# Optimization experiments

Hardware: AMD Instinct MI355X
Metric: run time of the kernel (lower is better)

Reference implementation:

```python
import jax, jax.numpy as jnp
import numpy as np

TOP_K = 2  # num_experts_per_token


def setup_inputs() -> dict:
    key = jax.random.key(0)
    k1, k2, k3, k4 = jax.random.split(key, 4)
    B, S, D, F, E = 2, 2048, 1024, 4096, 8
    hidden_states = jax.random.normal(k1, (B, S, D), dtype=jnp.float32)
    # router: nn.Linear(D, E, bias=False) -> weight [E, D]
    Wr = jax.random.normal(k2, (E, D), dtype=jnp.float32) * (1.0 / np.sqrt(D))
    # expert FFNs: W1 [E, D, F] (first Linear, transposed), W2 [E, F, D]
    W1 = jax.random.normal(k3, (E, D, F), dtype=jnp.float32) * (1.0 / np.sqrt(D))
    W2 = jax.random.normal(k4, (E, F, D), dtype=jnp.float32) * (1.0 / np.sqrt(F))
    return {"hidden_states": hidden_states, "Wr": Wr, "W1": W1, "W2": W2}


def reference(hidden_states, Wr, W1, W2):
    B, S, D = hidden_states.shape
    E = Wr.shape[0]
    x = hidden_states.reshape(-1, D)                      # [T, D]
    T = x.shape[0]

    router_logits = x @ Wr.T                              # [T, E]
    routing_weights = jax.nn.softmax(router_logits, axis=-1)
    top_w, top_idx = jax.lax.top_k(routing_weights, TOP_K)  # [T, K]
    top_w = top_w / jnp.sum(top_w, axis=-1, keepdims=True)

    # combine weights scattered into dense [T, E] (zero for unselected experts)
    comb = jnp.zeros((T, E), dtype=x.dtype).at[
        jnp.arange(T)[:, None], top_idx
    ].add(top_w)

    # per-expert FFN: SiLU(x @ W1) @ W2, computed densely then masked-combined
    h = jax.nn.silu(jnp.einsum('td,edf->tef', x, W1))     # [T, E, F]
    y = jnp.einsum('tef,efd->ted', h, W2)                 # [T, E, D]
    out = jnp.einsum('te,ted->td', comb, y)               # [T, D]
    return out.reshape(B, S, D)
```

## Files before the change

kernel.cpp:

```cpp
#include <hip/hip_runtime.h>
#include <hip/hip_bf16.h>

#define T_TOK 4096
#define DDIM  1024
#define FDIM  4096
#define NEXP  8
#define TLMAX 72

typedef __attribute__((ext_vector_type(8))) short bf16x8;
typedef __attribute__((ext_vector_type(4))) float f32x4;

__device__ __forceinline__ void gl2lds16(const void* g, void* l) {
  __builtin_amdgcn_global_load_lds((const __attribute__((address_space(1))) void*)g,
                                   (__attribute__((address_space(3))) void*)l,
                                   16, 0, 0);
}

__device__ __forceinline__ unsigned short f2bf(float f) {
  unsigned u = __float_as_uint(f);
  unsigned r = (u + 0x7fffu + ((u >> 16) & 1u)) >> 16;
  return (unsigned short)r;
}
__device__ __forceinline__ float bf2f(unsigned short u) {
  return __uint_as_float((unsigned)u << 16);
}

__global__ __launch_bounds__(256) void moe_router(
    const float* __restrict__ x, const float* __restrict__ Wr,
    unsigned short* __restrict__ xb, int* __restrict__ te, float* __restrict__ tw) {
  __shared__ float wr[NEXP * DDIM];
  const int tid = threadIdx.x;
#pragma unroll
  for (int i = 0; i < NEXP * DDIM / 256; ++i) wr[i * 256 + tid] = Wr[i * 256 + tid];
  __syncthreads();

  const int wave = tid >> 6, lane = tid & 63;
  const int t = blockIdx.x * 4 + wave;
  const float* xr = x + (size_t)t * DDIM;
  const int d0 = lane * 16;

  float4 xv[4];
#pragma unroll
  for (int j = 0; j < 4; ++j) xv[j] = *(const float4*)(xr + d0 + j * 4);

  float lg[NEXP];
#pragma unroll
  for (int e = 0; e < NEXP; ++e) {
    float s = 0.f;
#pragma unroll
    for (int j = 0; j < 4; ++j) {
      float4 wv = *(const float4*)(&wr[e * DDIM + d0 + j * 4]);
      s += xv[j].x * wv.x + xv[j].y * wv.y + xv[j].z * wv.z + xv[j].w * wv.w;
    }
    lg[e] = s;
  }
#pragma unroll
  for (int e = 0; e < NEXP; ++e) {
#pragma unroll
    for (int off = 32; off > 0; off >>= 1) lg[e] += __shfl_xor(lg[e], off);
  }

#pragma unroll
  for (int j = 0; j < 4; ++j) {
    ushort4 o;
    o.x = f2bf(xv[j].x); o.y = f2bf(xv[j].y); o.z = f2bf(xv[j].z); o.w = f2bf(xv[j].w);
    *(ushort4*)(xb + (size_t)t * DDIM + d0 + j * 4) = o;
  }

  if (lane == 0) {
    int i0 = 0;
#pragma unroll
    for (int e = 1; e < NEXP; ++e) if (lg[e] > lg[i0]) i0 = e;
    int i1 = (i0 == 0) ? 1 : 0;
#pragma unroll
    for (int e = 0; e < NEXP; ++e) if (e != i0 && lg[e] > lg[i1]) i1 = e;
    float w0 = 1.f / (1.f + __expf(lg[i1] - lg[i0]));
    te[t * 2 + 0] = i0; te[t * 2 + 1] = i1;
    tw[t * 2 + 0] = w0; tw[t * 2 + 1] = 1.f - w0;
  }
}

__global__ __launch_bounds__(256) void moe_count(const int* __restrict__ te,
                                                 int* __restrict__ counts) {
  __shared__ int lh[NEXP];
  const int tid = threadIdx.x;
  if (tid < NEXP) lh[tid] = 0;
  __syncthreads();
  const int t = blockIdx.x * 256 + tid;
  atomicAdd(&lh[te[t * 2 + 0]], 1);
  atomicAdd(&lh[te[t * 2 + 1]], 1);
  __syncthreads();
  if (tid < NEXP) atomicAdd(&counts[tid], lh[tid]);
}

__global__ void moe_prefix(const int* __restrict__ counts, int* __restrict__ offs,
                           int* __restrict__ fill, int* __restrict__ tcnt,
                           int* __restrict__ tlist) {
  if (threadIdx.x == 0) {
    int s = 0, tt = 0;
    for (int e = 0; e < NEXP; ++e) {
      offs[e] = s;
      int c = counts[e];
      s += c;
      fill[e] = 0;
      for (int mt = 0; mt * 128 < c; ++mt) tlist[tt++] = (e << 8) | mt;
    }
    offs[NEXP] = s;
    tcnt[0] = tt;
  }
}

__global__ __launch_bounds__(256) void moe_scatter(
    const int* __restrict__ te, const int* __restrict__ offs, int* __restrict__ fill,
    int* __restrict__ rows, int* __restrict__ slot) {
  __shared__ int lcnt[NEXP], lbase[NEXP];
  const int tid = threadIdx.x;
  if (tid < NEXP) lcnt[tid] = 0;
  __syncthreads();
  const int t = blockIdx.x * 256 + tid;
  const int e0 = te[t * 2 + 0], e1 = te[t * 2 + 1];
  const int r0 = atomicAdd(&lcnt[e0], 1);
  const int r1 = atomicAdd(&lcnt[e1], 1);
  __syncthreads();
  if (tid < NEXP) lbase[tid] = atomicAdd(&fill[tid], lcnt[tid]);
  __syncthreads();
  int p0 = offs[e0] + lbase[e0] + r0;
  int p1 = offs[e1] + lbase[e1] + r1;
  rows[p0] = t; rows[p1] = t;
  slot[t * 2 + 0] = p0; slot[t * 2 + 1] = p1;
}

__global__ __launch_bounds__(256) void wconv_t(const float* __restrict__ W,
                                               unsigned short* __restrict__ Wt,
                                               int K, int N) {
  __shared__ unsigned short t[64][65];
  const int e = blockIdx.z;
  const float* src = W + (size_t)e * K * N + (size_t)(blockIdx.y * 64) * N + blockIdx.x * 64;
  unsigned short* dst = Wt + (size_t)e * N * K + (size_t)(blockIdx.x * 64) * K + blockIdx.y * 64;
  const int tid = threadIdx.x;
  const int rr = tid >> 4;
  const int cc4 = (tid & 15) * 4;
#pragma unroll
  for (int i = 0; i < 4; ++i) {
    int r = i * 16 + rr;
    float4 v = *(const float4*)(src + (size_t)r * N + cc4);
    t[cc4 + 0][r] = f2bf(v.x);
    t[cc4 + 1][r] = f2bf(v.y);
    t[cc4 + 2][r] = f2bf(v.z);
    t[cc4 + 3][r] = f2bf(v.w);
  }
  __syncthreads();
  const int k8 = (tid & 7) * 8;
#pragma unroll
  for (int i = 0; i < 2; ++i) {
    int c = i * 32 + (tid >> 3);
    uint4 pk;
    pk.x = (unsigned)t[c][k8 + 0] | ((unsigned)t[c][k8 + 1] << 16);
    pk.y = (unsigned)t[c][k8 + 2] | ((unsigned)t[c][k8 + 3] << 16);
    pk.z = (unsigned)t[c][k8 + 4] | ((unsigned)t[c][k8 + 5] << 16);
    pk.w = (unsigned)t[c][k8 + 6] | ((unsigned)t[c][k8 + 7] << 16);
    *(uint4*)(dst + (size_t)c * K + k8) = pk;
  }
}

template <int KD, int KSLICE, int ND, bool GATHER, bool DOSILU>
__global__ __launch_bounds__(512, 4) void moe_gemm(
    const unsigned short* __restrict__ Asrc, const unsigned short* __restrict__ Wt,
    const int* __restrict__ rows, const int* __restrict__ offs,
    const int* __restrict__ tcnt, const int* __restrict__ tlist,
    unsigned short* __restrict__ Out) {
  constexpr int BM = 128, BN = 256, BK = 32;
  constexpr int S = KD / KSLICE;
  constexpr int NTN = ND / BN;
  constexpr int NPAN = NTN * S;
  constexpr int NB = TLMAX * NPAN;
  constexpr int MF = 4, NF = 4;

  __shared__ alignas(16) unsigned short Alds[2][BM * BK];
  __shared__ alignas(16) unsigned short Blds[2][BN * BK];

  const int bid = blockIdx.x;
  const int orig = (bid & 7) * (NB >> 3) + (bid >> 3);
  const int TT = tcnt[0];
  if (orig >= TT * NPAN) return;
  const int tt = orig % TT;
  const int panel = orig / TT;
  const int nt = panel % NTN;
  const int ksl = panel / NTN;
  const int pk = tlist[tt];
  const int e = pk >> 8, mt = pk & 255;

  const int base = offs[e];
  const int cnt = offs[e + 1] - base;
  const int m0 = mt * BM;
  const int valid = min(BM, cnt - m0);
  const size_t koff = (size_t)ksl * KSLICE;

  const int tid = threadIdx.x;
  const int w = tid >> 6, lane = tid & 63;
  const int wm = w >> 2, wn = w & 3;

  const int n0 = nt * BN;
  const unsigned short* Wb = Wt + (size_t)e * ND * KD + (size_t)n0 * KD + koff;

  const int cc8 = (((tid & 3) ^ ((tid >> 3) & 3)) * 8);
  const int ar = tid >> 2;
  const int aslot = base + m0 + min(ar, valid - 1);
  const size_t aoff = (size_t)(GATHER ? rows[aslot] : aslot) * KD + koff + cc8;
  size_t boff[2];
#pragma unroll
  for (int s = 0; s < 2; ++s) boff[s] = (size_t)(s * 128 + ar) * KD + cc8;

  f32x4 acc[MF][NF] = {};

#define STAGE(b, k0)                                                         \
  {                                                                          \
    gl2lds16(Asrc + aoff + (k0), &Alds[b][tid * 8]);                         \
    _Pragma("unroll") for (int s = 0; s < 2; ++s)                            \
        gl2lds16(Wb + boff[s] + (k0), &Blds[b][(s * 512 + tid) * 8]);        \
  }

#define COMPUTE(b)                                                           \
  {                                                                          \
    bf16x8 af[MF], bfr[NF];                                                  \
    _Pragma("unroll") for (int mf = 0; mf < MF; ++mf) {                      \
      int row = wm * 64 + mf * 16 + (lane & 15);                             \
      int cc = (lane >> 4) ^ ((row >> 1) & 3);                               \
      af[mf] = *(const bf16x8*)((const char*)&Alds[b][0] + row * 64 + cc * 16); \
    }                                                                        \
    _Pragma("unroll") for (int nf = 0; nf < NF; ++nf) {                      \
      int col = wn * 64 + nf * 16 + (lane & 15);                             \
      int cc = (lane >> 4) ^ ((col >> 1) & 3);                               \
      bfr[nf] = *(const bf16x8*)((const char*)&Blds[b][0] + col * 64 + cc * 16); \
    }                                                                        \
    _Pragma("unroll") for (int mf = 0; mf < MF; ++mf)                        \
        _Pragma("unroll") for (int nf = 0; nf < NF; ++nf)                    \
            acc[mf][nf] = __builtin_amdgcn_mfma_f32_16x16x32_bf16(           \
                af[mf], bfr[nf], acc[mf][nf], 0, 0, 0);                      \
  }

  constexpr int NK = KSLICE / BK;
  STAGE(0, 0);
  for (int t = 0; t < NK; t += 2) {
    STAGE(1, (t + 1) * BK);
    asm volatile("s_waitcnt vmcnt(3)" ::: "memory");
    __builtin_amdgcn_s_barrier();
    COMPUTE(0);
    __builtin_amdgcn_s_barrier();
    if (t + 2 < NK) {
      STAGE(0, (t + 2) * BK);
      asm volatile("s_waitcnt vmcnt(3)" ::: "memory");
    } else {
      asm volatile("s_waitcnt vmcnt(0)" ::: "memory");
    }
    __builtin_amdgcn_s_barrier();
    COMPUTE(1);
    __builtin_amdgcn_s_barrier();
  }
#undef STAGE
#undef COMPUTE

  unsigned short* Op = Out + (size_t)ksl * 8192 * ND;
  const int q = lane >> 4, c16 = lane & 15;
#pragma unroll
  for (int mf = 0; mf < MF; ++mf) {
#pragma unroll
    for (int r = 0; r < 4; ++r) {
      int lrow = wm * 64 + mf * 16 + q * 4 + r;
      if (lrow < valid) {
#pragma unroll
        for (int nf = 0; nf < NF; ++nf) {
          int gcol = n0 + wn * 64 + nf * 16 + c16;
          float v = acc[mf][nf][r];
          if (DOSILU) v = v / (1.f + __expf(-v));
          Op[(size_t)(base + m0 + lrow) * ND + gcol] = f2bf(v);
        }
      }
    }
  }
}

__global__ __launch_bounds__(256) void moe_combine(
    const unsigned short* __restrict__ y, const int* __restrict__ slot,
    const float* __restrict__ tw, float* __restrict__ out) {
  const int t = blockIdx.x;
  const int s0 = slot[t * 2], s1 = slot[t * 2 + 1];
  const float w0 = tw[t * 2], w1 = tw[t * 2 + 1];
  const int i = threadIdx.x * 4;
  ushort4 a = *(const ushort4*)(y + (size_t)s0 * DDIM + i);
  ushort4 b = *(const ushort4*)(y + (size_t)(8192 + s0) * DDIM + i);
  ushort4 c = *(const ushort4*)(y + (size_t)s1 * DDIM + i);
  ushort4 d = *(const ushort4*)(y + (size_t)(8192 + s1) * DDIM + i);
  float4 r;
  r.x = w0 * (bf2f(a.x) + bf2f(b.x)) + w1 * (bf2f(c.x) + bf2f(d.x));
  r.y = w0 * (bf2f(a.y) + bf2f(b.y)) + w1 * (bf2f(c.y) + bf2f(d.y));
  r.z = w0 * (bf2f(a.z) + bf2f(b.z)) + w1 * (bf2f(c.z) + bf2f(d.z));
  r.w = w0 * (bf2f(a.w) + bf2f(b.w)) + w1 * (bf2f(c.w) + bf2f(d.w));
  *(float4*)(out + (size_t)t * DDIM + i) = r;
}

extern "C" void kernel_launch(void* const* d_in, const int* in_sizes, int n_in,
                              void* d_out, int out_size, void* d_ws, size_t ws_size,
                              hipStream_t stream) {
  const float* x  = (const float*)d_in[0];
  const float* Wr = (const float*)d_in[1];
  const float* W1 = (const float*)d_in[2];
  const float* W2 = (const float*)d_in[3];
  float* out = (float*)d_out;

  char* ws = (char*)d_ws;
  unsigned short* xb = (unsigned short*)ws;
  unsigned short* H  = (unsigned short*)(ws + (size_t)(8 << 20));
  unsigned short* WT = (unsigned short*)(ws + (size_t)(72 << 20));
  unsigned short* y  = (unsigned short*)(ws + (size_t)(136 << 20));
  char* meta = ws + (size_t)(168 << 20);
  int* rows   = (int*)meta;
  int* te     = (int*)(meta + (32 << 10));
  float* tw   = (float*)(meta + (64 << 10));
  int* slot   = (int*)(meta + (96 << 10));
  int* counts = (int*)(meta + (128 << 10));
  int* offs   = counts + 16;
  int* fill   = counts + 32;
  int* tcnt   = counts + 48;
  int* tlist  = counts + 64;

  hipMemsetAsync(counts, 0, 256, stream);

  moe_router<<<T_TOK / 4, 256, 0, stream>>>(x, Wr, xb, te, tw);
  moe_count<<<T_TOK / 256, 256, 0, stream>>>(te, counts);
  moe_prefix<<<1, 64, 0, stream>>>(counts, offs, fill, tcnt, tlist);
  moe_scatter<<<T_TOK / 256, 256, 0, stream>>>(te, offs, fill, rows, slot);

  wconv_t<<<dim3(FDIM / 64, DDIM / 64, NEXP), 256, 0, stream>>>(W1, WT, DDIM, FDIM);
  moe_gemm<DDIM, DDIM, FDIM, true, true>
      <<<TLMAX * (FDIM / 256), 512, 0, stream>>>(xb, WT, rows, offs, tcnt, tlist, H);

  wconv_t<<<dim3(DDIM / 64, FDIM / 64, NEXP), 256, 0, stream>>>(W2, WT, FDIM, DDIM);
  moe_gemm<FDIM, FDIM / 2, DDIM, false, false>
      <<<TLMAX * (DDIM / 256) * 2, 512, 0, stream>>>(H, WT, nullptr, offs, tcnt, tlist, y);

  moe_combine<<<T_TOK, 256, 0, stream>>>(y, slot, tw, out);
}
```

Before: 318.7 us.

## Deepen MoE GEMM LDS pipeline to four stages with interleaved prefetch

Replaces the double-buffered LDS pipeline with a four-slot ring buffer, processing two BK=32 sub-tiles per loop iteration. Each phase loads its fragments, issues the next global-to-LDS prefetch, then runs the MFMAs at raised wave priority. The LDS swizzle is changed to a three-term XOR to reduce bank conflicts. Occupancy hint drops from 4 to 2 blocks per CU because LDS use doubles, trading latency hiding across blocks for deeper prefetch within a block.

```diff
diff --git a/kernel.cpp b/kernel.cpp
--- a/kernel.cpp
+++ b/kernel.cpp
@@ -164,20 +164,20 @@
 }
 
 template <int KD, int KSLICE, int ND, bool GATHER, bool DOSILU>
-__global__ __launch_bounds__(512, 4) void moe_gemm(
+__global__ __launch_bounds__(512, 2) void moe_gemm(
     const unsigned short* __restrict__ Asrc, const unsigned short* __restrict__ Wt,
     const int* __restrict__ rows, const int* __restrict__ offs,
     const int* __restrict__ tcnt, const int* __restrict__ tlist,
     unsigned short* __restrict__ Out) {
-  constexpr int BM = 128, BN = 256, BK = 32;
+  constexpr int BM = 128, BN = 256;
+  constexpr int NK = KSLICE / 64;
   constexpr int S = KD / KSLICE;
   constexpr int NTN = ND / BN;
   constexpr int NPAN = NTN * S;
   constexpr int NB = TLMAX * NPAN;
-  constexpr int MF = 4, NF = 4;
-
-  __shared__ alignas(16) unsigned short Alds[2][BM * BK];
-  __shared__ alignas(16) unsigned short Blds[2][BN * BK];
+
+  __shared__ alignas(16) unsigned short Ards[4 * BM * 32];
+  __shared__ alignas(16) unsigned short Brds[4 * BN * 32];
 
   const int bid = blockIdx.x;
   const int orig = (bid & 7) * (NB >> 3) + (bid >> 3);
@@ -203,7 +203,7 @@
   const int n0 = nt * BN;
   const unsigned short* Wb = Wt + (size_t)e * ND * KD + (size_t)n0 * KD + koff;
 
-  const int cc8 = (((tid & 3) ^ ((tid >> 3) & 3)) * 8);
+  const int cc8 = (((tid & 3) ^ ((tid >> 2) & 3) ^ ((tid >> 4) & 3)) * 8);
   const int ar = tid >> 2;
   const int aslot = base + m0 + min(ar, valid - 1);
   const size_t aoff = (size_t)(GATHER ? rows[aslot] : aslot) * KD + koff + cc8;
@@ -211,65 +211,65 @@
 #pragma unroll
   for (int s = 0; s < 2; ++s) boff[s] = (size_t)(s * 128 + ar) * KD + cc8;
 
-  f32x4 acc[MF][NF] = {};
-
-#define STAGE(b, k0)                                                         \
-  {                                                                          \
-    gl2lds16(Asrc + aoff + (k0), &Alds[b][tid * 8]);                         \
-    _Pragma("unroll") for (int s = 0; s < 2; ++s)                            \
-        gl2lds16(Wb + boff[s] + (k0), &Blds[b][(s * 512 + tid) * 8]);        \
-  }
-
-#define COMPUTE(b)                                                           \
-  {                                                                          \
-    bf16x8 af[MF], bfr[NF];                                                  \
-    _Pragma("unroll") for (int mf = 0; mf < MF; ++mf) {                      \
-      int row = wm * 64 + mf * 16 + (lane & 15);                             \
-      int cc = (lane >> 4) ^ ((row >> 1) & 3);                               \
-      af[mf] = *(const bf16x8*)((const char*)&Alds[b][0] + row * 64 + cc * 16); \
-    }                                                                        \
-    _Pragma("unroll") for (int nf = 0; nf < NF; ++nf) {                      \
-      int col = wn * 64 + nf * 16 + (lane & 15);                             \
-      int cc = (lane >> 4) ^ ((col >> 1) & 3);                               \
-      bfr[nf] = *(const bf16x8*)((const char*)&Blds[b][0] + col * 64 + cc * 16); \
-    }                                                                        \
-    _Pragma("unroll") for (int mf = 0; mf < MF; ++mf)                        \
-        _Pragma("unroll") for (int nf = 0; nf < NF; ++nf)                    \
-            acc[mf][nf] = __builtin_amdgcn_mfma_f32_16x16x32_bf16(           \
-                af[mf], bfr[nf], acc[mf][nf], 0, 0, 0);                      \
-  }
-
-  constexpr int NK = KSLICE / BK;
-  STAGE(0, 0);
+  const int kgp = (lane >> 4) ^ (lane & 3) ^ ((lane >> 2) & 3);
+  const int aro = (wm * 64 + (lane & 15)) * 64 + kgp * 16;
+  const int bro = (wn * 64 + (lane & 15)) * 64 + kgp * 16;
+
+  f32x4 acc[4][4] = {};
+
+#define SA(sl, ke) gl2lds16(Asrc + aoff + (ke), Ards + (sl)*4096 + tid * 8)
+#define SB(sl, ke, s) gl2lds16(Wb + boff[s] + (ke), Brds + (sl)*8192 + ((s)*512 + tid) * 8)
+
+#define PHASE(sl, STG)                                                        \
+  {                                                                           \
+    bf16x8 af[4], bfr[4];                                                     \
+    const char* Ab = (const char*)Ards + (sl) * 8192 + aro;                   \
+    const char* Bb = (const char*)Brds + (sl) * 16384 + bro;                  \
+    _Pragma("unroll") for (int mf = 0; mf < 4; ++mf)                          \
+        af[mf] = *(const bf16x8*)(Ab + mf * 1024);                            \
+    _Pragma("unroll") for (int nf = 0; nf < 4; ++nf)                          \
+        bfr[nf] = *(const bf16x8*)(Bb + nf * 1024);                           \
+    STG;                                                                      \
+    asm volatile("s_waitcnt vmcnt(6)" ::: "memory");                          \
+    __builtin_amdgcn_s_barrier();                                             \
+    __builtin_amdgcn_s_setprio(1);                                            \
+    _Pragma("unroll") for (int mf = 0; mf < 4; ++mf)                          \
+        _Pragma("unroll") for (int nf = 0; nf < 4; ++nf)                      \
+            acc[mf][nf] = __builtin_amdgcn_mfma_f32_16x16x32_bf16(            \
+                af[mf], bfr[nf], acc[mf][nf], 0, 0, 0);                       \
+    __builtin_amdgcn_s_setprio(0);                                            \
+    __builtin_amdgcn_s_barrier();                                             \
+  }
+
+  SA(0, 0); SB(0, 0, 0); SB(0, 0, 1);
+  SA(1, 32); SB(1, 32, 0); SB(1, 32, 1);
+  SA(2, 64); SB(2, 64, 0); SB(2, 64, 1);
+  asm volatile("s_waitcnt vmcnt(6)" ::: "memory");
+  __syncthreads();
+
   for (int t = 0; t < NK; t += 2) {
-    STAGE(1, (t + 1) * BK);
-    asm volatile("s_waitcnt vmcnt(3)" ::: "memory");
-    __builtin_amdgcn_s_barrier();
-    COMPUTE(0);
-    __builtin_amdgcn_s_barrier();
-    if (t + 2 < NK) {
-      STAGE(0, (t + 2) * BK);
-      asm volatile("s_waitcnt vmcnt(3)" ::: "memory");
-    } else {
-      asm volatile("s_waitcnt vmcnt(0)" ::: "memory");
-    }
-    __builtin_amdgcn_s_barrier();
-    COMPUTE(1);
-    __builtin_amdgcn_s_barrier();
-  }
-#undef STAGE
-#undef COMPUTE
+    const int k1 = min(t + 1, NK - 1) * 64 + 32;
+    const int k2 = min(t + 2, NK - 1) * 64;
+    const int k3 = min(t + 3, NK - 1) * 64;
+    PHASE(0, { SB(3, k1, 0); SB(3, k1, 1); SA(3, k1); });
+    PHASE(1, { SA(0, k2); SB(0, k2, 0); SB(0, k2, 1); });
+    PHASE(2, { SB(1, k2 + 32, 0); SB(1, k2 + 32, 1); SA(1, k2 + 32); });
+    PHASE(3, { SA(2, k3); SB(2, k3, 0); SB(2, k3, 1); });
+  }
+#undef PHASE
+#undef SA
+#undef SB
 
   unsigned short* Op = Out + (size_t)ksl * 8192 * ND;
   const int q = lane >> 4, c16 = lane & 15;
 #pragma unroll
-  for (int mf = 0; mf < MF; ++mf) {
+  for (int mf = 0; mf < 4; ++mf) {
 #pragma unroll
     for (int r = 0; r < 4; ++r) {
       int lrow = wm * 64 + mf * 16 + q * 4 + r;
       if (lrow < valid) {
 #pragma unroll
-        for (int nf = 0; nf < NF; ++nf) {
+        for (int nf = 0; nf < 4; ++nf) {
           int gcol = n0 + wn * 64 + nf * 16 + c16;
           float v = acc[mf][nf][r];
           if (DOSILU) v = v / (1.f + __expf(-v));
```

New measurement: 337.0 us. 1.06x slower.

## Add 256x256-tile first expert GEMM with 4-stage LDS pipeline

Applied to the files above, without the earlier changes.

Replaces the generic 128x256-tile first GEMM with a dedicated kernel that computes 256x256 output tiles per block. It uses a 4-slot LDS ring with loads issued two steps ahead, split barriers and MFMA priority hints. A second tile list at 256-row granularity is built in the prefix kernel. Larger tiles cut weight re-reads per token and raise MFMA density, at the cost of more LDS (128KB), lower occupancy (2 blocks/CU), more padding waste on partial expert tiles, and fewer blocks to spread across CUs.

```diff
diff --git a/kernel.cpp b/kernel.cpp
--- a/kernel.cpp
+++ b/kernel.cpp
@@ -6,6 +6,7 @@
 #define FDIM  4096
 #define NEXP  8
 #define TLMAX 72
+#define TL2MAX 40
 
 typedef __attribute__((ext_vector_type(8))) short bf16x8;
 typedef __attribute__((ext_vector_type(4))) float f32x4;
@@ -95,18 +96,20 @@
 
 __global__ void moe_prefix(const int* __restrict__ counts, int* __restrict__ offs,
                            int* __restrict__ fill, int* __restrict__ tcnt,
-                           int* __restrict__ tlist) {
+                           int* __restrict__ tlist, int* __restrict__ tlist2) {
   if (threadIdx.x == 0) {
-    int s = 0, tt = 0;
+    int s = 0, tt = 0, t2 = 0;
     for (int e = 0; e < NEXP; ++e) {
       offs[e] = s;
       int c = counts[e];
       s += c;
       fill[e] = 0;
       for (int mt = 0; mt * 128 < c; ++mt) tlist[tt++] = (e << 8) | mt;
+      for (int mt = 0; mt * 256 < c; ++mt) tlist2[t2++] = (e << 8) | mt;
     }
     offs[NEXP] = s;
     tcnt[0] = tt;
+    tcnt[1] = t2;
   }
 }
 
@@ -160,6 +163,122 @@
     pk.z = (unsigned)t[c][k8 + 4] | ((unsigned)t[c][k8 + 5] << 16);
     pk.w = (unsigned)t[c][k8 + 6] | ((unsigned)t[c][k8 + 7] << 16);
     *(uint4*)(dst + (size_t)c * K + k8) = pk;
+  }
+}
+
+__global__ __launch_bounds__(512, 2) void moe_gemm1(
+    const unsigned short* __restrict__ Asrc, const unsigned short* __restrict__ Wt,
+    const int* __restrict__ rows, const int* __restrict__ offs,
+    const int* __restrict__ tcnt, const int* __restrict__ tlist2,
+    unsigned short* __restrict__ Hout) {
+  constexpr int KD = DDIM, ND = FDIM;
+  constexpr int NTN = ND / 256;
+  constexpr int NB = TL2MAX * NTN;
+  constexpr int NK = KD / 32;
+
+  __shared__ alignas(16) unsigned short As[4][256 * 32];
+  __shared__ alignas(16) unsigned short Bs[4][256 * 32];
+
+  const int bid = blockIdx.x;
+  const int orig = (bid & 7) * (NB >> 3) + (bid >> 3);
+  const int TT = tcnt[1];
+  if (orig >= TT * NTN) return;
+  const int tt = orig % TT;
+  const int nt = orig / TT;
+  const int pk = tlist2[tt];
+  const int e = pk >> 8, mt = pk & 255;
+
+  const int base = offs[e];
+  const int cnt = offs[e + 1] - base;
+  const int m0 = mt * 256;
+  const int valid = min(256, cnt - m0);
+
+  const int tid = threadIdx.x;
+  const int w = tid >> 6, lane = tid & 63;
+  const int wm = w >> 2, wn = w & 3;
+
+  const int n0 = nt * 256;
+  const unsigned short* Wb = Wt + (size_t)e * (size_t)ND * KD + (size_t)n0 * KD;
+
+  const int cc8 = ((tid & 3) ^ ((tid >> 3) & 3)) * 8;
+  const int ar = tid >> 2;
+  size_t aoff[2], boff[2];
+#pragma unroll
+  for (int s = 0; s < 2; ++s) {
+    int r = s * 128 + ar;
+    int sl = base + m0 + min(r, valid - 1);
+    aoff[s] = (size_t)rows[sl] * KD + cc8;
+    boff[s] = (size_t)r * KD + cc8;
+  }
+
+  const int rc = (lane >> 4) ^ (((lane & 15) >> 1) & 3);
+  const int aro = (wm * 128 + (lane & 15)) * 64 + rc * 16;
+  const int bro = (wn * 64 + (lane & 15)) * 64 + rc * 16;
+
+  f32x4 acc[8][4] = {};
+
+#define SA1(sl, ke, s) gl2lds16(Asrc + aoff[s] + (ke), &As[sl][(s * 512 + tid) * 8])
+#define SB1(sl, ke, s) gl2lds16(Wb + boff[s] + (ke), &Bs[sl][(s * 512 + tid) * 8])
+
+  SA1(0, 0, 0); SA1(0, 0, 1); SB1(0, 0, 0); SB1(0, 0, 1);
+  SA1(1, 32, 0); SA1(1, 32, 1); SB1(1, 32, 0); SB1(1, 32, 1);
+  asm volatile("s_waitcnt vmcnt(4)" ::: "memory");
+  __syncthreads();
+
+  for (int t = 0; t < NK; ++t) {
+    const int sl = t & 3;
+    const int s2 = (t + 2) & 3;
+    const int k2 = min(t + 2, NK - 1) * 32;
+    const char* Ab = (const char*)&As[sl][0] + aro;
+    const char* Bb = (const char*)&Bs[sl][0] + bro;
+    bf16x8 af[4], bfr[4];
+#pragma unroll
+    for (int mf = 0; mf < 4; ++mf) af[mf] = *(const bf16x8*)(Ab + mf * 1024);
+#pragma unroll
+    for (int nf = 0; nf < 4; ++nf) bfr[nf] = *(const bf16x8*)(Bb + nf * 1024);
+    SA1(s2, k2, 0); SA1(s2, k2, 1);
+    __builtin_amdgcn_s_barrier();
+    __builtin_amdgcn_s_setprio(1);
+#pragma unroll
+    for (int mf = 0; mf < 4; ++mf)
+#pragma unroll
+      for (int nf = 0; nf < 4; ++nf)
+        acc[mf][nf] = __builtin_amdgcn_mfma_f32_16x16x32_bf16(af[mf], bfr[nf], acc[mf][nf], 0, 0, 0);
+    __builtin_amdgcn_s_setprio(0);
+    __builtin_amdgcn_s_barrier();
+#pragma unroll
+    for (int mf = 0; mf < 4; ++mf) af[mf] = *(const bf16x8*)(Ab + (mf + 4) * 1024);
+    SB1(s2, k2, 0); SB1(s2, k2, 1);
+    asm volatile("s_waitcnt vmcnt(4)" ::: "memory");
+    __builtin_amdgcn_s_barrier();
+    __builtin_amdgcn_s_setprio(1);
+#pragma unroll
+    for (int mf = 0; mf < 4; ++mf)
+#pragma unroll
+      for (int nf = 0; nf < 4; ++nf)
+        acc[mf + 4][nf] = __builtin_amdgcn_mfma_f32_16x16x32_bf16(af[mf], bfr[nf], acc[mf + 4][nf], 0, 0, 0);
+    __builtin_amdgcn_s_setprio(0);
+    __builtin_amdgcn_s_barrier();
+  }
+#undef SA1
+#undef SB1
+
+  const int q = lane >> 4, c16 = lane & 15;
+#pragma unroll
+  for (int mf = 0; mf < 8; ++mf) {
+#pragma unroll
+    for (int r = 0; r < 4; ++r) {
+      int lrow = wm * 128 + mf * 16 + q * 4 + r;
+      if (lrow < valid) {
+#pragma unroll
+        for (int nf = 0; nf < 4; ++nf) {
+          int gcol = n0 + wn * 64 + nf * 16 + c16;
+          float v = acc[mf][nf][r];
+          v = v / (1.f + __expf(-v));
+          Hout[(size_t)(base + m0 + lrow) * ND + gcol] = f2bf(v);
+        }
+      }
+    }
   }
 }
 
@@ -323,17 +442,17 @@
   int* fill   = counts + 32;
   int* tcnt   = counts + 48;
   int* tlist  = counts + 64;
-
-  hipMemsetAsync(counts, 0, 256, stream);
+  int* tlist2 = counts + 192;
+
+  hipMemsetAsync(counts, 0, 1024, stream);
 
   moe_router<<<T_TOK / 4, 256, 0, stream>>>(x, Wr, xb, te, tw);
   moe_count<<<T_TOK / 256, 256, 0, stream>>>(te, counts);
-  moe_prefix<<<1, 64, 0, stream>>>(counts, offs, fill, tcnt, tlist);
+  moe_prefix<<<1, 64, 0, stream>>>(counts, offs, fill, tcnt, tlist, tlist2);
   moe_scatter<<<T_TOK / 256, 256, 0, stream>>>(te, offs, fill, rows, slot);
 
   wconv_t<<<dim3(FDIM / 64, DDIM / 64, NEXP), 256, 0, stream>>>(W1, WT, DDIM, FDIM);
-  moe_gemm<DDIM, DDIM, FDIM, true, true>
-      <<<TLMAX * (FDIM / 256), 512, 0, stream>>>(xb, WT, rows, offs, tcnt, tlist, H);
+  moe_gemm1<<<TL2MAX * (FDIM / 256), 512, 0, stream>>>(xb, WT, rows, offs, tcnt, tlist2, H);
 
   wconv_t<<<dim3(DDIM / 64, FDIM / 64, NEXP), 256, 0, stream>>>(W2, WT, FDIM, DDIM);
   moe_gemm<FDIM, FDIM / 2, DDIM, false, false>
```

New measurement: 347.4 us. 9.0% more time.

## Retile MoE GEMM to 256x128 blocks with 4 waves of 128x64 each

Applied to the files above, without the earlier changes.

The expert GEMM moves from 128x256 tiles run by 8 waves to 256x128 tiles run by 4 waves. Each wave now computes a 128x64 sub-tile with 32 accumulators, and the token-tile list is rebuilt in 256-row chunks. The aim is more MFMA work per LDS fragment load and fewer tiles per expert. In exchange, occupancy drops, register pressure rises, and padding waste grows on partially filled expert tiles.

```diff
diff --git a/kernel.cpp b/kernel.cpp
--- a/kernel.cpp
+++ b/kernel.cpp
@@ -5,7 +5,7 @@
 #define DDIM  1024
 #define FDIM  4096
 #define NEXP  8
-#define TLMAX 72
+#define TL2MAX 40
 
 typedef __attribute__((ext_vector_type(8))) short bf16x8;
 typedef __attribute__((ext_vector_type(4))) float f32x4;
@@ -95,18 +95,18 @@
 
 __global__ void moe_prefix(const int* __restrict__ counts, int* __restrict__ offs,
                            int* __restrict__ fill, int* __restrict__ tcnt,
-                           int* __restrict__ tlist) {
+                           int* __restrict__ tlist2) {
   if (threadIdx.x == 0) {
-    int s = 0, tt = 0;
+    int s = 0, t2 = 0;
     for (int e = 0; e < NEXP; ++e) {
       offs[e] = s;
       int c = counts[e];
       s += c;
       fill[e] = 0;
-      for (int mt = 0; mt * 128 < c; ++mt) tlist[tt++] = (e << 8) | mt;
+      for (int mt = 0; mt * 256 < c; ++mt) tlist2[t2++] = (e << 8) | mt;
     }
     offs[NEXP] = s;
-    tcnt[0] = tt;
+    tcnt[1] = t2;
   }
 }
 
@@ -164,30 +164,29 @@
 }
 
 template <int KD, int KSLICE, int ND, bool GATHER, bool DOSILU>
-__global__ __launch_bounds__(512, 4) void moe_gemm(
+__global__ __launch_bounds__(256, 2) void moe_gemm(
     const unsigned short* __restrict__ Asrc, const unsigned short* __restrict__ Wt,
     const int* __restrict__ rows, const int* __restrict__ offs,
-    const int* __restrict__ tcnt, const int* __restrict__ tlist,
+    const int* __restrict__ tcnt, const int* __restrict__ tlist2,
     unsigned short* __restrict__ Out) {
-  constexpr int BM = 128, BN = 256, BK = 32;
+  constexpr int BM = 256, BN = 128, BK = 32;
   constexpr int S = KD / KSLICE;
   constexpr int NTN = ND / BN;
   constexpr int NPAN = NTN * S;
-  constexpr int NB = TLMAX * NPAN;
-  constexpr int MF = 4, NF = 4;
+  constexpr int NB = TL2MAX * NPAN;
 
   __shared__ alignas(16) unsigned short Alds[2][BM * BK];
   __shared__ alignas(16) unsigned short Blds[2][BN * BK];
 
   const int bid = blockIdx.x;
   const int orig = (bid & 7) * (NB >> 3) + (bid >> 3);
-  const int TT = tcnt[0];
+  const int TT = tcnt[1];
   if (orig >= TT * NPAN) return;
   const int tt = orig % TT;
   const int panel = orig / TT;
   const int nt = panel % NTN;
   const int ksl = panel / NTN;
-  const int pk = tlist[tt];
+  const int pk = tlist2[tt];
   const int e = pk >> 8, mt = pk & 255;
 
   const int base = offs[e];
@@ -198,58 +197,73 @@
 
   const int tid = threadIdx.x;
   const int w = tid >> 6, lane = tid & 63;
-  const int wm = w >> 2, wn = w & 3;
+  const int wm = w >> 1, wn = w & 1;
 
   const int n0 = nt * BN;
   const unsigned short* Wb = Wt + (size_t)e * ND * KD + (size_t)n0 * KD + koff;
 
-  const int cc8 = (((tid & 3) ^ ((tid >> 3) & 3)) * 8);
+  const int cc8 = ((tid & 3) ^ ((tid >> 3) & 3)) * 8;
   const int ar = tid >> 2;
-  const int aslot = base + m0 + min(ar, valid - 1);
-  const size_t aoff = (size_t)(GATHER ? rows[aslot] : aslot) * KD + koff + cc8;
-  size_t boff[2];
-#pragma unroll
-  for (int s = 0; s < 2; ++s) boff[s] = (size_t)(s * 128 + ar) * KD + cc8;
-
-  f32x4 acc[MF][NF] = {};
-
-#define STAGE(b, k0)                                                         \
-  {                                                                          \
-    gl2lds16(Asrc + aoff + (k0), &Alds[b][tid * 8]);                         \
-    _Pragma("unroll") for (int s = 0; s < 2; ++s)                            \
-        gl2lds16(Wb + boff[s] + (k0), &Blds[b][(s * 512 + tid) * 8]);        \
-  }
-
-#define COMPUTE(b)                                                           \
-  {                                                                          \
-    bf16x8 af[MF], bfr[NF];                                                  \
-    _Pragma("unroll") for (int mf = 0; mf < MF; ++mf) {                      \
-      int row = wm * 64 + mf * 16 + (lane & 15);                             \
-      int cc = (lane >> 4) ^ ((row >> 1) & 3);                               \
-      af[mf] = *(const bf16x8*)((const char*)&Alds[b][0] + row * 64 + cc * 16); \
-    }                                                                        \
-    _Pragma("unroll") for (int nf = 0; nf < NF; ++nf) {                      \
-      int col = wn * 64 + nf * 16 + (lane & 15);                             \
-      int cc = (lane >> 4) ^ ((col >> 1) & 3);                               \
-      bfr[nf] = *(const bf16x8*)((const char*)&Blds[b][0] + col * 64 + cc * 16); \
-    }                                                                        \
-    _Pragma("unroll") for (int mf = 0; mf < MF; ++mf)                        \
-        _Pragma("unroll") for (int nf = 0; nf < NF; ++nf)                    \
-            acc[mf][nf] = __builtin_amdgcn_mfma_f32_16x16x32_bf16(           \
-                af[mf], bfr[nf], acc[mf][nf], 0, 0, 0);                      \
+  size_t aoff[4], boff[2];
+#pragma unroll
+  for (int s = 0; s < 4; ++s) {
+    int r = s * 64 + ar;
+    int sl = base + m0 + min(r, valid - 1);
+    aoff[s] = (size_t)(GATHER ? rows[sl] : sl) * KD + koff + cc8;
+  }
+#pragma unroll
+  for (int s = 0; s < 2; ++s) boff[s] = (size_t)(s * 64 + ar) * KD + cc8;
+
+  const int rc = (lane >> 4) ^ (((lane & 15) >> 1) & 3);
+  const int aro = (wm * 128 + (lane & 15)) * 64 + rc * 16;
+  const int bro = (wn * 64 + (lane & 15)) * 64 + rc * 16;
+
+  f32x4 acc[8][4] = {};
+
+#define STAGE(b, k0)                                                          \
+  {                                                                           \
+    _Pragma("unroll") for (int s = 0; s < 4; ++s)                             \
+        gl2lds16(Asrc + aoff[s] + (k0), &Alds[b][(s * 256 + tid) * 8]);       \
+    _Pragma("unroll") for (int s = 0; s < 2; ++s)                             \
+        gl2lds16(Wb + boff[s] + (k0), &Blds[b][(s * 256 + tid) * 8]);         \
+  }
+
+#define COMPUTE(b)                                                            \
+  {                                                                           \
+    bf16x8 bfr[4];                                                            \
+    _Pragma("unroll") for (int nf = 0; nf < 4; ++nf)                          \
+        bfr[nf] = *(const bf16x8*)((const char*)&Blds[b][0] + bro + nf * 1024); \
+    {                                                                         \
+      bf16x8 af[4];                                                           \
+      _Pragma("unroll") for (int mf = 0; mf < 4; ++mf)                        \
+          af[mf] = *(const bf16x8*)((const char*)&Alds[b][0] + aro + mf * 1024); \
+      _Pragma("unroll") for (int mf = 0; mf < 4; ++mf)                        \
+          _Pragma("unroll") for (int nf = 0; nf < 4; ++nf)                    \
+              acc[mf][nf] = __builtin_amdgcn_mfma_f32_16x16x32_bf16(          \
+                  af[mf], bfr[nf], acc[mf][nf], 0, 0, 0);                     \
+    }                                                                         \
+    {                                                                         \
+      bf16x8 af[4];                                                           \
+      _Pragma("unroll") for (int mf = 0; mf < 4; ++mf)                        \
+          af[mf] = *(const bf16x8*)((const char*)&Alds[b][0] + aro + (mf + 4) * 1024); \
+      _Pragma("unroll") for (int mf = 0; mf < 4; ++mf)                        \
+          _Pragma("unroll") for (int nf = 0; nf < 4; ++nf)                    \
+              acc[mf + 4][nf] = __builtin_amdgcn_mfma_f32_16x16x32_bf16(      \
+                  af[mf], bfr[nf], acc[mf + 4][nf], 0, 0, 0);                 \
+    }                                                                         \
   }
 
   constexpr int NK = KSLICE / BK;
   STAGE(0, 0);
   for (int t = 0; t < NK; t += 2) {
     STAGE(1, (t + 1) * BK);
-    asm volatile("s_waitcnt vmcnt(3)" ::: "memory");
+    asm volatile("s_waitcnt vmcnt(6)" ::: "memory");
     __builtin_amdgcn_s_barrier();
     COMPUTE(0);
     __builtin_amdgcn_s_barrier();
     if (t + 2 < NK) {
       STAGE(0, (t + 2) * BK);
-      asm volatile("s_waitcnt vmcnt(3)" ::: "memory");
+      asm volatile("s_waitcnt vmcnt(6)" ::: "memory");
     } else {
       asm volatile("s_waitcnt vmcnt(0)" ::: "memory");
     }
@@ -263,13 +277,13 @@
   unsigned short* Op = Out + (size_t)ksl * 8192 * ND;
   const int q = lane >> 4, c16 = lane & 15;
 #pragma unroll
-  for (int mf = 0; mf < MF; ++mf) {
+  for (int mf = 0; mf < 8; ++mf) {
 #pragma unroll
     for (int r = 0; r < 4; ++r) {
-      int lrow = wm * 64 + mf * 16 + q * 4 + r;
+      int lrow = wm * 128 + mf * 16 + q * 4 + r;
       if (lrow < valid) {
 #pragma unroll
-        for (int nf = 0; nf < NF; ++nf) {
+        for (int nf = 0; nf < 4; ++nf) {
           int gcol = n0 + wn * 64 + nf * 16 + c16;
           float v = acc[mf][nf][r];
           if (DOSILU) v = v / (1.f + __expf(-v));
@@ -322,22 +336,22 @@
   int* offs   = counts + 16;
   int* fill   = counts + 32;
   int* tcnt   = counts + 48;
-  int* tlist  = counts + 64;
-
-  hipMemsetAsync(counts, 0, 256, stream);
+  int* tlist2 = counts + 64;
+
+  hipMemsetAsync(counts, 0, 1024, stream);
 
   moe_router<<<T_TOK / 4, 256, 0, stream>>>(x, Wr, xb, te, tw);
   moe_count<<<T_TOK / 256, 256, 0, stream>>>(te, counts);
-  moe_prefix<<<1, 64, 0, stream>>>(counts, offs, fill, tcnt, tlist);
+  moe_prefix<<<1, 64, 0, stream>>>(counts, offs, fill, tcnt, tlist2);
   moe_scatter<<<T_TOK / 256, 256, 0, stream>>>(te, offs, fill, rows, slot);
 
   wconv_t<<<dim3(FDIM / 64, DDIM / 64, NEXP), 256, 0, stream>>>(W1, WT, DDIM, FDIM);
   moe_gemm<DDIM, DDIM, FDIM, true, true>
-      <<<TLMAX * (FDIM / 256), 512, 0, stream>>>(xb, WT, rows, offs, tcnt, tlist, H);
+      <<<TL2MAX * (FDIM / 128), 256, 0, stream>>>(xb, WT, rows, offs, tcnt, tlist2, H);
 
   wconv_t<<<dim3(DDIM / 64, FDIM / 64, NEXP), 256, 0, stream>>>(W2, WT, FDIM, DDIM);
   moe_gemm<FDIM, FDIM / 2, DDIM, false, false>
-      <<<TLMAX * (DDIM / 256) * 2, 512, 0, stream>>>(H, WT, nullptr, offs, tcnt, tlist, y);
+      <<<TL2MAX * (DDIM / 128) * 2, 256, 0, stream>>>(H, WT, nullptr, offs, tcnt, tlist2, y);
 
   moe_combine<<<T_TOK, 256, 0, stream>>>(y, slot, tw, out);
 }
```

Result: slower. 368.6 us (+15.6%).
